# Performance work log

Hardware: AMD Instinct MI355X
Metric: run time of the kernel (lower is better)

## Reference

```python
import jax, jax.numpy as jnp
import numpy as np

B, N, DIM = 4, 1024, 2048
H, HKV, D = 16, 4, 128          # n_heads, n_kv_heads, head_dim
CACHE = 3072                     # cached KV length
WINDOW = 2048                    # max_window_len (sliding window)
EPS = 1e-6


def setup_inputs() -> dict:
    key = jax.random.key(0)
    ks = jax.random.split(key, 10)
    x = jax.random.normal(ks[0], (B, N, DIM), dtype=jnp.float32)
    past_k = jax.random.normal(ks[1], (B, HKV, CACHE, D), dtype=jnp.float32)
    past_v = jax.random.normal(ks[2], (B, HKV, CACHE, D), dtype=jnp.float32)
    # RoPE angles for the current segment (absolute positions CACHE..CACHE+N-1),
    # matching MultiLevelRoPE 'face' level: freqs = 1/theta**(arange(0,D,2)/D)
    pos = jnp.arange(CACHE, CACHE + N, dtype=jnp.float32)
    inv_freq = 1.0 / (10000.0 ** (jnp.arange(0, D, 2, dtype=jnp.float32) / D))
    ang = pos[:, None] * inv_freq[None, :]          # [N, D//2]
    freqs_cos = jnp.cos(ang)
    freqs_sin = jnp.sin(ang)
    s = 0.02
    Wq = jax.random.normal(ks[3], (H * D, DIM), dtype=jnp.float32) * s
    Wk = jax.random.normal(ks[4], (HKV * D, DIM), dtype=jnp.float32) * s
    Wv = jax.random.normal(ks[5], (HKV * D, DIM), dtype=jnp.float32) * s
    Wo = jax.random.normal(ks[6], (DIM, H * D), dtype=jnp.float32) * s
    bo = jnp.zeros((DIM,), dtype=jnp.float32)
    wq_norm = jnp.ones((D,), dtype=jnp.float32)
    wk_norm = jnp.ones((D,), dtype=jnp.float32)
    return {"x": x, "past_k": past_k, "past_v": past_v,
            "freqs_cos": freqs_cos, "freqs_sin": freqs_sin,
            "Wq": Wq, "Wk": Wk, "Wv": Wv, "Wo": Wo, "bo": bo,
            "wq_norm": wq_norm, "wk_norm": wk_norm}


def _rms_norm(t, w):
    # torch.nn.RMSNorm over head_dim
    return t * jax.lax.rsqrt(jnp.mean(t * t, axis=-1, keepdims=True) + EPS) * w


def _rope(t, cos, sin):
    # interleaved-pair complex rotation, as in MultiLevelRoPE.apply
    # t: [B, h, N, D]; cos/sin: [N, D//2]
    t2 = t.reshape(*t.shape[:-1], D // 2, 2)
    x0, x1 = t2[..., 0], t2[..., 1]
    c = cos[None, None, :, :]
    s = sin[None, None, :, :]
    r0 = x0 * c - x1 * s
    r1 = x0 * s + x1 * c
    return jnp.stack([r0, r1], axis=-1).reshape(t.shape)


def reference(x, past_k, past_v, freqs_cos, freqs_sin,
              Wq, Wk, Wv, Wo, bo, wq_norm, wk_norm):
    # projections -> [B, h, N, D]
    q = (x @ Wq.T).reshape(B, N, H, D).transpose(0, 2, 1, 3)
    k = (x @ Wk.T).reshape(B, N, HKV, D).transpose(0, 2, 1, 3)
    v = (x @ Wv.T).reshape(B, N, HKV, D).transpose(0, 2, 1, 3)
    # qk rms_norm on head_dim
    q = _rms_norm(q, wq_norm)
    k = _rms_norm(k, wk_norm)
    # RoPE on current segment (cached K already rotated)
    q = _rope(q, freqs_cos, freqs_sin)
    k = _rope(k, freqs_cos, freqs_sin)
    # append to cache -> M = CACHE + N
    k_all = jnp.concatenate([past_k, k], axis=2)   # [B, HKV, M, D]
    v_all = jnp.concatenate([past_v, v], axis=2)
    # repeat_kv for GQA
    n_rep = H // HKV
    k_rep = jnp.repeat(k_all, n_rep, axis=1)       # [B, H, M, D]
    v_rep = jnp.repeat(v_all, n_rep, axis=1)
    M = CACHE + N
    scale = 1.0 / jnp.sqrt(jnp.asarray(D, dtype=q.dtype))
    scores = jnp.einsum('bhnd,bhmd->bhnm', q, k_rep) * scale
    # causal + sliding-window mask over absolute positions
    qpos = jnp.arange(N) + CACHE                   # [N]
    kpos = jnp.arange(M)                           # [M]
    allowed = (kpos[None, :] <= qpos[:, None]) & (qpos[:, None] - kpos[None, :] < WINDOW)
    scores = jnp.where(allowed[None, None], scores, jnp.asarray(-1e30, dtype=scores.dtype))
    probs = jax.nn.softmax(scores, axis=-1)
    attn = jnp.einsum('bhnm,bhmd->bhnd', probs, v_rep)
    attn = attn.transpose(0, 2, 1, 3).reshape(B, N, H * D)
    return attn @ Wo.T + bo
```

## Files before the change

kernel.cpp:

```cpp
#include <hip/hip_runtime.h>
#include <hip/hip_bf16.h>
#include <stdint.h>

typedef unsigned short u16;
typedef unsigned int u32;
typedef __attribute__((ext_vector_type(8))) __bf16 bfrag;
typedef __attribute__((ext_vector_type(4))) float f32x4;
typedef __attribute__((ext_vector_type(16))) float f32x16;
typedef __attribute__((ext_vector_type(4))) unsigned short u16x4;

__device__ __forceinline__ u16 f2bf(float f){
  union { float f; u32 u; } v; v.f = f;
  u32 u = v.u;
  return (u16)((u + 0x7fffu + ((u >> 16) & 1u)) >> 16);
}

__device__ __forceinline__ u32 cvtpk(float a, float b){
  u32 r; asm("v_cvt_pk_bf16_f32 %0, %1, %2" : "=v"(r) : "v"(a), "v"(b)); return r;
}
__device__ __forceinline__ void swap32(u32 &a, u32 &b){
  asm volatile("v_permlane32_swap_b32 %0, %1" : "+v"(a), "+v"(b));
}

__device__ __forceinline__ void gload_lds16(const void* g, void* l){
  __builtin_amdgcn_global_load_lds(
      (__attribute__((address_space(1))) void*)(unsigned long long)g,
      (__attribute__((address_space(3))) void*)(u32)(unsigned long long)l,
      16, 0, 0);
}

__global__ void __launch_bounds__(256) k_cvt(const float* __restrict__ s, u16* __restrict__ d, int n4){
  int i = blockIdx.x*256 + threadIdx.x;
  if (i >= n4) return;
  float4 v = ((const float4*)s)[i];
  u16x4 o; o[0]=f2bf(v.x); o[1]=f2bf(v.y); o[2]=f2bf(v.z); o[3]=f2bf(v.w);
  ((u16x4*)d)[i] = o;
}

__global__ void __launch_bounds__(256) k_cvt_past(const float* __restrict__ s, u16* __restrict__ d, int n4){
  int i = blockIdx.x*256 + threadIdx.x;
  if (i >= n4) return;
  int e = i*4;
  int row = e >> 7;
  int col = e & 127;
  int bh = row / 3072;
  int m = row - bh*3072;
  float4 v = ((const float4*)s)[i];
  u16x4 o; o[0]=f2bf(v.x); o[1]=f2bf(v.y); o[2]=f2bf(v.z); o[3]=f2bf(v.w);
  *(u16x4*)(d + ((size_t)(bh*4096 + m) << 7) + col) = o;
}

__global__ void __launch_bounds__(256) k_cvt_past_vt(const float* __restrict__ s, u16* __restrict__ v_t){
  __shared__ u16 T[64][65];
  const int mt = blockIdx.x, dt = blockIdx.y, pl = blockIdx.z;
  const float* src = s + (size_t)pl*3072*128 + (size_t)mt*64*128 + dt*64;
  u16* dst = v_t + (size_t)pl*128*4096 + (size_t)dt*64*4096 + mt*64;
  const int t = threadIdx.x;
  #pragma unroll
  for (int r = 0; r < 2; ++r){
    int row = r*32 + (t >> 3);
    int c8 = (t & 7)*8;
    float4 va = *(const float4*)(src + (size_t)row*128 + c8);
    float4 vb = *(const float4*)(src + (size_t)row*128 + c8 + 4);
    T[row][c8+0]=f2bf(va.x); T[row][c8+1]=f2bf(va.y); T[row][c8+2]=f2bf(va.z); T[row][c8+3]=f2bf(va.w);
    T[row][c8+4]=f2bf(vb.x); T[row][c8+5]=f2bf(vb.y); T[row][c8+6]=f2bf(vb.z); T[row][c8+7]=f2bf(vb.w);
  }
  __syncthreads();
  #pragma unroll
  for (int r = 0; r < 2; ++r){
    int drow = r*32 + (t >> 3);
    int m8 = (t & 7)*8;
    union { bfrag v; u16 e[8]; } uv;
    #pragma unroll
    for (int j = 0; j < 8; ++j) uv.e[j] = T[m8 + j][drow];
    *(bfrag*)(dst + (size_t)drow*4096 + m8) = uv.v;
  }
}

template<int EPI>
__global__ void __launch_bounds__(256) k_gemm(
    const u16* __restrict__ A, const u16* __restrict__ Bm,
    u16* __restrict__ Cb, float* __restrict__ Cf, const float* __restrict__ bias,
    int M, int Nn, int K)
{
  __shared__ u16 lsA[2][4096];
  __shared__ u16 lsB[2][4096];
  const int t = threadIdx.x, lane = t & 63, wid = t >> 6;
  const int l15 = lane & 15, l4 = lane >> 4;
  const int wm = wid >> 1, wn = wid & 1;
  const int bn = blockIdx.x, bm = blockIdx.y;
  const u16* Ab = A + (size_t)bm*128*K;
  const u16* Bb = Bm + (size_t)bn*128*K;

  auto stage = [&](u16* ls, const u16* g, int kof){
    #pragma unroll
    for (int r = 0; r < 2; ++r){
      int row = r*64 + (t >> 2);
      int s = (t & 3) ^ ((row >> 1) & 3);
      gload_lds16(g + (size_t)row*K + kof + s*8, ls + r*2048 + wid*512);
    }
  };

  f32x4 acc[4][4] = {};
  stage(&lsA[0][0], Ab, 0);
  stage(&lsB[0][0], Bb, 0);
  const int NT = K >> 5;
  const int sl = l4 ^ ((l15 >> 1) & 3);
  const int ra0 = wm*64 + l15, rb0 = wn*64 + l15;
  for (int kt = 0; kt < NT; ++kt){
    __syncthreads();
    const int cur = kt & 1;
    if (kt + 1 < NT){
      stage(&lsA[cur ^ 1][0], Ab, (kt + 1)*32);
      stage(&lsB[cur ^ 1][0], Bb, (kt + 1)*32);
    }
    bfrag af[4], bfv[4];
    #pragma unroll
    for (int i = 0; i < 4; ++i){
      af[i]  = *(const bfrag*)&lsA[cur][(ra0 + i*16)*32 + sl*8];
      bfv[i] = *(const bfrag*)&lsB[cur][(rb0 + i*16)*32 + sl*8];
    }
    #pragma unroll
    for (int i = 0; i < 4; ++i)
      #pragma unroll
      for (int j = 0; j < 4; ++j)
        acc[i][j] = __builtin_amdgcn_mfma_f32_16x16x32_bf16(af[i], bfv[j], acc[i][j], 0, 0, 0);
  }
  const int row0 = bm*128 + wm*64, col0 = bn*128 + wn*64;
  #pragma unroll
  for (int i = 0; i < 4; ++i)
    #pragma unroll
    for (int j = 0; j < 4; ++j){
      int cc = col0 + j*16 + l15;
      float bv = (EPI == 1) ? bias[cc] : 0.f;
      #pragma unroll
      for (int r = 0; r < 4; ++r){
        int rr = row0 + i*16 + l4*4 + r;
        if (EPI == 0) Cb[(size_t)rr*Nn + cc] = f2bf(acc[i][j][r]);
        else          Cf[(size_t)rr*Nn + cc] = acc[i][j][r] + bv;
      }
    }
}

__global__ void __launch_bounds__(256) k_rmsrope(
    const u16* __restrict__ proj, const float* __restrict__ cosb, const float* __restrict__ sinb,
    const float* __restrict__ wq, const float* __restrict__ wk,
    u16* __restrict__ q_ro, u16* __restrict__ k_all, u16* __restrict__ v_all)
{
  const int bn = blockIdx.x;
  const int b = bn >> 10, n = bn & 1023;
  const int lane = threadIdx.x & 63, w = threadIdx.x >> 6;
  const int chunk = blockIdx.y*4 + w;
  const u16* src = proj + (size_t)bn*3072 + chunk*128 + lane*2;
  const u32 raw = *(const u32*)src;
  union { u32 u; float f; } a, c2;
  a.u = raw << 16; c2.u = raw & 0xffff0000u;
  float x0 = a.f, x1 = c2.f;
  if (chunk >= 20){
    int hk = chunk - 20;
    *(u32*)(v_all + (((size_t)(b*4 + hk)*4096 + 3072 + n) << 7) + lane*2) = raw;
    return;
  }
  float ss = x0*x0 + x1*x1;
  #pragma unroll
  for (int m = 1; m < 64; m <<= 1) ss += __shfl_xor(ss, m, 64);
  float inv = rsqrtf(ss*(1.f/128.f) + 1e-6f);
  const float* wn2 = (chunk < 16) ? wq : wk;
  x0 *= inv*wn2[lane*2]; x1 *= inv*wn2[lane*2 + 1];
  float cz = cosb[n*64 + lane], sz = sinb[n*64 + lane];
  float r0 = x0*cz - x1*sz;
  float r1 = x0*sz + x1*cz;
  if (chunk < 16){
    const float KLF = 0.127529904f;
    r0 *= KLF; r1 *= KLF;
    u32 outp = (u32)f2bf(r0) | ((u32)f2bf(r1) << 16);
    *(u32*)(q_ro + (((size_t)(b*16 + chunk)*1024 + n) << 7) + lane*2) = outp;
  } else {
    int hk = chunk - 16;
    u32 outp = (u32)f2bf(r0) | ((u32)f2bf(r1) << 16);
    *(u32*)(k_all + (((size_t)(b*4 + hk)*4096 + 3072 + n) << 7) + lane*2) = outp;
  }
}

__global__ void __launch_bounds__(256) k_transpose_v(const u16* __restrict__ v_all, u16* __restrict__ v_t){
  __shared__ u16 T[64][65];
  const int mt = blockIdx.x + 48, dt = blockIdx.y, pl = blockIdx.z;
  const u16* src = v_all + (size_t)pl*4096*128 + (size_t)mt*64*128 + dt*64;
  u16* dst = v_t + (size_t)pl*128*4096 + (size_t)dt*64*4096 + mt*64;
  const int t = threadIdx.x;
  #pragma unroll
  for (int r = 0; r < 2; ++r){
    int row = r*32 + (t >> 3);
    int c8 = (t & 7)*8;
    bfrag v = *(const bfrag*)(src + (size_t)row*128 + c8);
    union { bfrag v; u16 e[8]; } uv; uv.v = v;
    #pragma unroll
    for (int j = 0; j < 8; ++j) T[row][c8 + j] = uv.e[j];
  }
  __syncthreads();
  #pragma unroll
  for (int r = 0; r < 2; ++r){
    int drow = r*32 + (t >> 3);
    int m8 = (t & 7)*8;
    union { bfrag v; u16 e[8]; } uv;
    #pragma unroll
    for (int j = 0; j < 8; ++j) uv.e[j] = T[m8 + j][drow];
    *(bfrag*)(dst + (size_t)drow*4096 + m8) = uv.v;
  }
}

__global__ void __launch_bounds__(512, 4) k_attn(
    const u16* __restrict__ q_ro, const u16* __restrict__ k_all,
    const u16* __restrict__ v_t, u16* __restrict__ attn_o)
{
  __shared__ u16 smem[32768];
  __shared__ float Lsh[4][32];
  const int bid = blockIdx.x;
  const int xcd = bid & 7, idx = bid >> 3;
  const int plane = (xcd << 1) | (idx >> 5);
  const int qt = idx & 31;
  const int b = plane >> 2, hk = plane & 3;
  const int t = threadIdx.x, lane = t & 63, w = t >> 6;
  const int l31 = lane & 31, lh = lane >> 5;
  const int hf = w >> 2;
  const int hd = w & 3;
  const int h = hk*4 + hd;
  const int qbase = qt*32;

  const u16* qplane = q_ro + (size_t)(b*16 + h)*1024*128;
  const u16* kplane = k_all + (size_t)(b*4 + hk)*4096*128;
  const u16* vplane = v_t  + (size_t)(b*4 + hk)*128*4096;

  bfrag qf[8];
  {
    const u16* qrow = qplane + (size_t)(qbase + l31)*128 + lh*8;
    #pragma unroll
    for (int dks = 0; dks < 8; ++dks)
      qf[dks] = *(const bfrag*)(qrow + dks*16);
  }

  const int krow = t >> 4, kslot = t & 15;
  const int koff0 = krow*128 + ((kslot ^ (krow & 7))*8);
  const int vrow = t >> 3, vslot = t & 7;
  const int voff0 = vrow*4096 + ((vslot ^ (vrow & 7))*8);

  const int swb = (lh << 4) ^ ((l31 & 7) << 4);
  const int kaddr = (hf*32 + l31)*256 + swb;
  const int vaddr = l31*128 + swb;

  const int kb0 = (qbase + 1024) & ~63;
  const int qpos = 3072 + qbase + l31;
  const char* smb = (const char*)smem;

  f32x16 acc_o[4] = {};
  float l_run = 0.f;

  {
    const u16* kc = kplane + (size_t)kb0*128;
    const u16* vc = vplane + kb0;
    gload_lds16(kc + koff0,          smem + t*8);
    gload_lds16(kc + koff0 + 4096,   smem + 4096 + t*8);
    gload_lds16(vc + voff0,          smem + 16384 + t*8);
    gload_lds16(vc + voff0 + 262144, smem + 20480 + t*8);
  }

  for (int c = 0; c < 33; ++c){
    __syncthreads();
    const int cur = c & 1;
    if (c < 32){
      const u16* kc = kplane + (size_t)(kb0 + (c + 1)*64)*128;
      const u16* vc = vplane + kb0 + (c + 1)*64;
      u16* kd = smem + (cur ^ 1)*8192;
      u16* vd = smem + 16384 + (cur ^ 1)*8192;
      gload_lds16(kc + koff0,          kd + t*8);
      gload_lds16(kc + koff0 + 4096,   kd + 4096 + t*8);
      gload_lds16(vc + voff0,          vd + t*8);
      gload_lds16(vc + voff0 + 262144, vd + 4096 + t*8);
    }

    const int kaddrB = kaddr + cur*16384;
    const int vaddrB = vaddr + cur*16384;

    f32x16 s = {};
    __builtin_amdgcn_s_setprio(1);
    #pragma unroll
    for (int dks = 0; dks < 8; ++dks){
      bfrag kf = *(const bfrag*)(smb + (kaddrB ^ (dks << 5)));
      s = __builtin_amdgcn_mfma_f32_32x32x16_bf16(kf, qf[dks], s, 0, 0, 0);
    }
    __builtin_amdgcn_s_setprio(0);

    if ((c == 0) | (c == 32)){
      const int kb = kb0 + c*64;
      #pragma unroll
      for (int r = 0; r < 16; ++r){
        int kpos = kb + hf*32 + (r & 3) + 8*(r >> 2) + 4*lh;
        int dq = qpos - kpos;
        if ((unsigned)dq >= 2048u) s[r] = -1e30f;
      }
    }

    #pragma unroll
    for (int r = 0; r < 16; ++r) s[r] = exp2f(s[r]);
    {
      float a0 = (s[0]+s[1]) + (s[2]+s[3]);
      float a1 = (s[4]+s[5]) + (s[6]+s[7]);
      float a2 = (s[8]+s[9]) + (s[10]+s[11]);
      float a3 = (s[12]+s[13]) + (s[14]+s[15]);
      float lc = (a0 + a1) + (a2 + a3);
      lc += __shfl_xor(lc, 32, 64);
      l_run += lc;
    }

    union { u32 u[4]; bfrag v; } pf[2];
    {
      u32 a0 = cvtpk(s[0],  s[1]),  a1 = cvtpk(s[2],  s[3]);
      u32 b0 = cvtpk(s[4],  s[5]),  b1 = cvtpk(s[6],  s[7]);
      swap32(a0, b0); swap32(a1, b1);
      pf[0].u[0]=a0; pf[0].u[1]=a1; pf[0].u[2]=b0; pf[0].u[3]=b1;
      u32 c0 = cvtpk(s[8],  s[9]),  c1 = cvtpk(s[10], s[11]);
      u32 e0 = cvtpk(s[12], s[13]), e1 = cvtpk(s[14], s[15]);
      swap32(c0, e0); swap32(c1, e1);
      pf[1].u[0]=c0; pf[1].u[1]=c1; pf[1].u[2]=e0; pf[1].u[3]=e1;
    }

    __builtin_amdgcn_s_setprio(1);
    #pragma unroll
    for (int lks = 0; lks < 2; ++lks){
      const int va = vaddrB ^ ((hf*2 + lks) << 5);
      #pragma unroll
      for (int dj = 0; dj < 4; ++dj){
        bfrag vf = *(const bfrag*)(smb + 32768 + va + dj*4096);
        acc_o[dj] = __builtin_amdgcn_mfma_f32_32x32x16_bf16(vf, pf[lks].v, acc_o[dj], 0, 0, 0);
      }
    }
    __builtin_amdgcn_s_setprio(0);
  }

  __syncthreads();
  float* Om = (float*)smem;
  if (hf == 1){
    if (lh == 0) Lsh[hd][l31] = l_run;
    #pragma unroll
    for (int dj = 0; dj < 4; ++dj)
      #pragma unroll
      for (int rg = 0; rg < 4; ++rg){
        int slot = dj*8 + rg*2 + lh;
        f32x4 vv;
        #pragma unroll
        for (int j = 0; j < 4; ++j) vv[j] = acc_o[dj][rg*4 + j];
        *(f32x4*)&Om[hd*4096 + l31*128 + ((slot ^ (l31 & 7)) << 2)] = vv;
      }
  }
  __syncthreads();
  if (hf == 0){
    float ltot = l_run + Lsh[hd][l31];
    float inv = 1.0f / ltot;
    const int bn = b*1024 + qbase + l31;
    u16* orow = attn_o + (size_t)bn*2048 + h*128;
    #pragma unroll
    for (int dj = 0; dj < 4; ++dj)
      #pragma unroll
      for (int rg = 0; rg < 4; ++rg){
        int slot = dj*8 + rg*2 + lh;
        f32x4 vv = *(const f32x4*)&Om[hd*4096 + l31*128 + ((slot ^ (l31 & 7)) << 2)];
        int d0 = dj*32 + rg*8 + lh*4;
        u16x4 o;
        #pragma unroll
        for (int j = 0; j < 4; ++j) o[j] = f2bf((acc_o[dj][rg*4 + j] + vv[j])*inv);
        *(u16x4*)(orow + d0) = o;
      }
  }
}

extern "C" void kernel_launch(void* const* d_in, const int* in_sizes, int n_in,
                              void* d_out, int out_size, void* d_ws, size_t ws_size,
                              hipStream_t stream)
{
  const float* x      = (const float*)d_in[0];
  const float* past_k = (const float*)d_in[1];
  const float* past_v = (const float*)d_in[2];
  const float* fcos   = (const float*)d_in[3];
  const float* fsin   = (const float*)d_in[4];
  const float* Wq     = (const float*)d_in[5];
  const float* Wk     = (const float*)d_in[6];
  const float* Wv     = (const float*)d_in[7];
  const float* Wo     = (const float*)d_in[8];
  const float* bo     = (const float*)d_in[9];
  const float* wqn    = (const float*)d_in[10];
  const float* wkn    = (const float*)d_in[11];
  float* out = (float*)d_out;
  char* ws = (char*)d_ws;

  u16* xb    = (u16*)(ws);
  u16* wqkv  = (u16*)(ws + 16777216);
  u16* wo_b  = (u16*)(ws + 29360128);
  u16* q_ro  = (u16*)(ws + 37748736);
  u16* k_all = (u16*)(ws + 54525952);
  u16* v_all = (u16*)(ws + 71303168);
  u16* v_t   = (u16*)(ws + 88080384);
  u16* proj  = (u16*)(ws + 104857600);
  u16* attn_o = proj;

  k_cvt<<<8192, 256, 0, stream>>>(x, xb, 2097152);
  k_cvt<<<4096, 256, 0, stream>>>(Wq, wqkv, 1048576);
  k_cvt<<<1024, 256, 0, stream>>>(Wk, wqkv + 2048*2048, 262144);
  k_cvt<<<1024, 256, 0, stream>>>(Wv, wqkv + 2560*2048, 262144);
  k_cvt<<<4096, 256, 0, stream>>>(Wo, wo_b, 1048576);
  k_cvt_past<<<6144, 256, 0, stream>>>(past_k, k_all, 1572864);
  k_cvt_past_vt<<<dim3(48, 2, 16), 256, 0, stream>>>(past_v, v_t);

  k_gemm<0><<<dim3(24, 32), 256, 0, stream>>>(xb, wqkv, proj, nullptr, nullptr, 4096, 3072, 2048);
  k_rmsrope<<<dim3(4096, 6), 256, 0, stream>>>(proj, fcos, fsin, wqn, wkn, q_ro, k_all, v_all);
  k_transpose_v<<<dim3(16, 2, 16), 256, 0, stream>>>(v_all, v_t);
  k_attn<<<512, 512, 0, stream>>>(q_ro, k_all, v_t, attn_o);
  k_gemm<1><<<dim3(16, 32), 256, 0, stream>>>(attn_o, wo_b, nullptr, out, bo, 4096, 2048, 2048);
}
```

Measured before the change: 265.7 us.

## Load K/V fragments directly from global into registers, dropping LDS staging

The attention kernel no longer stages K and V tiles through double-buffered shared memory with per-iteration block barriers. Each wave now loads its own MFMA operand fragments straight from global memory into registers and prefetches the next chunk right after the current MFMAs. Launch bounds drop to 2 blocks per CU to make room for the extra registers. This removes the per-chunk __syncthreads and LDS traffic. In exchange, the four head-waves sharing a KV head each read K/V from global (relying on cache), the V reads are strided, and occupancy is lower.

```diff
diff --git a/kernel.cpp b/kernel.cpp
--- a/kernel.cpp
+++ b/kernel.cpp
@@ -209,11 +209,11 @@
   }
 }
 
-__global__ void __launch_bounds__(512, 4) k_attn(
+__global__ void __launch_bounds__(512, 2) k_attn(
     const u16* __restrict__ q_ro, const u16* __restrict__ k_all,
     const u16* __restrict__ v_t, u16* __restrict__ attn_o)
 {
-  __shared__ u16 smem[32768];
+  __shared__ float Om[4][4096];
   __shared__ float Lsh[4][32];
   const int bid = blockIdx.x;
   const int xcd = bid & 7, idx = bid >> 3;
@@ -239,59 +239,45 @@
       qf[dks] = *(const bfrag*)(qrow + dks*16);
   }
 
-  const int krow = t >> 4, kslot = t & 15;
-  const int koff0 = krow*128 + ((kslot ^ (krow & 7))*8);
-  const int vrow = t >> 3, vslot = t & 7;
-  const int voff0 = vrow*4096 + ((vslot ^ (vrow & 7))*8);
-
-  const int swb = (lh << 4) ^ ((l31 & 7) << 4);
-  const int kaddr = (hf*32 + l31)*256 + swb;
-  const int vaddr = l31*128 + swb;
-
   const int kb0 = (qbase + 1024) & ~63;
   const int qpos = 3072 + qbase + l31;
-  const char* smb = (const char*)smem;
+
+  const u16* kbase0 = kplane + (hf*32 + l31)*128 + lh*8;
+  const u16* vbase0 = vplane + (size_t)l31*4096 + hf*32 + lh*8;
 
   f32x16 acc_o[4] = {};
   float l_run = 0.f;
 
+  bfrag kf[8], vf[8];
   {
-    const u16* kc = kplane + (size_t)kb0*128;
-    const u16* vc = vplane + kb0;
-    gload_lds16(kc + koff0,          smem + t*8);
-    gload_lds16(kc + koff0 + 4096,   smem + 4096 + t*8);
-    gload_lds16(vc + voff0,          smem + 16384 + t*8);
-    gload_lds16(vc + voff0 + 262144, smem + 20480 + t*8);
+    const u16* kb_p = kbase0 + (size_t)kb0*128;
+    #pragma unroll
+    for (int dks = 0; dks < 8; ++dks) kf[dks] = *(const bfrag*)(kb_p + dks*16);
+    const u16* vb_p = vbase0 + kb0;
+    #pragma unroll
+    for (int lks = 0; lks < 2; ++lks)
+      #pragma unroll
+      for (int dj = 0; dj < 4; ++dj)
+        vf[lks*4 + dj] = *(const bfrag*)(vb_p + (size_t)dj*131072 + lks*16);
   }
 
   for (int c = 0; c < 33; ++c){
-    __syncthreads();
-    const int cur = c & 1;
-    if (c < 32){
-      const u16* kc = kplane + (size_t)(kb0 + (c + 1)*64)*128;
-      const u16* vc = vplane + kb0 + (c + 1)*64;
-      u16* kd = smem + (cur ^ 1)*8192;
-      u16* vd = smem + 16384 + (cur ^ 1)*8192;
-      gload_lds16(kc + koff0,          kd + t*8);
-      gload_lds16(kc + koff0 + 4096,   kd + 4096 + t*8);
-      gload_lds16(vc + voff0,          vd + t*8);
-      gload_lds16(vc + voff0 + 262144, vd + 4096 + t*8);
-    }
-
-    const int kaddrB = kaddr + cur*16384;
-    const int vaddrB = vaddr + cur*16384;
+    const int kb = kb0 + c*64;
 
     f32x16 s = {};
     __builtin_amdgcn_s_setprio(1);
     #pragma unroll
-    for (int dks = 0; dks < 8; ++dks){
-      bfrag kf = *(const bfrag*)(smb + (kaddrB ^ (dks << 5)));
-      s = __builtin_amdgcn_mfma_f32_32x32x16_bf16(kf, qf[dks], s, 0, 0, 0);
-    }
+    for (int dks = 0; dks < 8; ++dks)
+      s = __builtin_amdgcn_mfma_f32_32x32x16_bf16(kf[dks], qf[dks], s, 0, 0, 0);
     __builtin_amdgcn_s_setprio(0);
 
+    if (c < 32){
+      const u16* kb_n = kbase0 + (size_t)(kb + 64)*128;
+      #pragma unroll
+      for (int dks = 0; dks < 8; ++dks) kf[dks] = *(const bfrag*)(kb_n + dks*16);
+    }
+
     if ((c == 0) | (c == 32)){
-      const int kb = kb0 + c*64;
       #pragma unroll
       for (int r = 0; r < 16; ++r){
         int kpos = kb + hf*32 + (r & 3) + 8*(r >> 2) + 4*lh;
@@ -326,19 +312,23 @@
 
     __builtin_amdgcn_s_setprio(1);
     #pragma unroll
-    for (int lks = 0; lks < 2; ++lks){
-      const int va = vaddrB ^ ((hf*2 + lks) << 5);
-      #pragma unroll
-      for (int dj = 0; dj < 4; ++dj){
-        bfrag vf = *(const bfrag*)(smb + 32768 + va + dj*4096);
-        acc_o[dj] = __builtin_amdgcn_mfma_f32_32x32x16_bf16(vf, pf[lks].v, acc_o[dj], 0, 0, 0);
-      }
-    }
+    for (int lks = 0; lks < 2; ++lks)
+      #pragma unroll
+      for (int dj = 0; dj < 4; ++dj)
+        acc_o[dj] = __builtin_amdgcn_mfma_f32_32x32x16_bf16(vf[lks*4 + dj], pf[lks].v, acc_o[dj], 0, 0, 0);
     __builtin_amdgcn_s_setprio(0);
+
+    if (c < 32){
+      const u16* vb_n = vbase0 + kb + 64;
+      #pragma unroll
+      for (int lks = 0; lks < 2; ++lks)
+        #pragma unroll
+        for (int dj = 0; dj < 4; ++dj)
+          vf[lks*4 + dj] = *(const bfrag*)(vb_n + (size_t)dj*131072 + lks*16);
+    }
   }
 
   __syncthreads();
-  float* Om = (float*)smem;
   if (hf == 1){
     if (lh == 0) Lsh[hd][l31] = l_run;
     #pragma unroll
@@ -349,7 +339,7 @@
         f32x4 vv;
         #pragma unroll
         for (int j = 0; j < 4; ++j) vv[j] = acc_o[dj][rg*4 + j];
-        *(f32x4*)&Om[hd*4096 + l31*128 + ((slot ^ (l31 & 7)) << 2)] = vv;
+        *(f32x4*)&Om[hd][l31*128 + ((slot ^ (l31 & 7)) << 2)] = vv;
       }
   }
   __syncthreads();
@@ -363,7 +353,7 @@
       #pragma unroll
       for (int rg = 0; rg < 4; ++rg){
         int slot = dj*8 + rg*2 + lh;
-        f32x4 vv = *(const f32x4*)&Om[hd*4096 + l31*128 + ((slot ^ (l31 & 7)) << 2)];
+        f32x4 vv = *(const f32x4*)&Om[hd][l31*128 + ((slot ^ (l31 & 7)) << 2)];
         int d0 = dj*32 + rg*8 + lh*4;
         u16x4 o;
         #pragma unroll
```

New measurement: 401.9 us. +51.3%, slower.
